# Kernel optimization log

Measured on AMD Instinct MI355X. Metric: run time of the kernel, lower is better.

Reference implementation:

```python
import jax, jax.numpy as jnp
import numpy as np

N_V, N_E, N_F = 6000, 12000, 8000
D_IN, D_OUT = 32, 32


def _glorot(key, shape):
    lim = float(np.sqrt(6.0 / (shape[0] + shape[1])))
    return jax.random.uniform(key, shape, jnp.float32, -lim, lim)


def setup_inputs() -> dict:
    key = jax.random.key(0)
    ks = jax.random.split(key, 13)
    return {
        "xv": jax.random.normal(ks[0], (N_V, D_IN), jnp.float32),
        "xe": jax.random.normal(ks[1], (N_E, D_IN), jnp.float32),
        "xf": jax.random.normal(ks[2], (N_F, D_IN), jnp.float32),
        "Gv2v": jax.random.normal(ks[3], (N_V, N_V), jnp.float32) / np.sqrt(N_V),
        "Gv2e": jax.random.normal(ks[4], (N_E, N_V), jnp.float32) / np.sqrt(N_V),
        "Ge2e": jax.random.normal(ks[5], (N_E, N_E), jnp.float32) / np.sqrt(N_E),
        "Ge2f": jax.random.normal(ks[6], (N_F, N_E), jnp.float32) / np.sqrt(N_E),
        "Gf2f": jax.random.normal(ks[7], (N_F, N_F), jnp.float32) / np.sqrt(N_F),
        "Wv2v": _glorot(ks[8], (D_IN, D_OUT)),
        "Wv2e": _glorot(ks[9], (D_IN, D_OUT)),
        "We2e": _glorot(ks[10], (D_IN, D_OUT)),
        "We2f": _glorot(ks[11], (D_IN, D_OUT)),
        "Wf2f": _glorot(ks[12], (D_IN, D_OUT)),
    }


def reference(xv, xe, xf, Gv2v, Gv2e, Ge2e, Ge2f, Gf2f,
              Wv2v, Wv2e, We2e, We2f, Wf2f):
    # Eval mode: dropout is identity. activation=None -> no nonlinearity.
    # LTN(x, G) = G @ (x @ W); MergeOper = sum of two LTNs.
    zv = Gv2v @ (xv @ Wv2v)                               # [n_v, d_out]
    ze = Gv2e @ (xv @ Wv2e) + Ge2e @ (xe @ We2e)          # [n_e, d_out]
    zf = Ge2f @ (xe @ We2f) + Gf2f @ (xf @ Wf2f)          # [n_f, d_out]
    return zv, ze, zf
```

## Files before the change

kernel.cpp:

```cpp
#include <hip/hip_runtime.h>

typedef float  f32x4 __attribute__((ext_vector_type(4)));
typedef short  s16x8 __attribute__((ext_vector_type(8)));

#define PK   256
#define PSTR 260
#define TM   32

typedef const __attribute__((address_space(1))) float* gas1f;
typedef __attribute__((address_space(3))) float*       las3f;

__device__ __forceinline__ short f2bf(float f) {
  unsigned u = __builtin_bit_cast(unsigned, f);
  u += 0x7FFFu + ((u >> 16) & 1u);
  return (short)(u >> 16);
}

__global__ __launch_bounds__(256) void build_yt(
    const float* __restrict__ xv, const float* __restrict__ xe,
    const float* __restrict__ xf,
    const float* __restrict__ Wv2v, const float* __restrict__ Wv2e,
    const float* __restrict__ We2e, const float* __restrict__ We2f,
    const float* __restrict__ Wf2f, short* __restrict__ Yt)
{
  int bid = blockIdx.x;
  const float* x; const float* W; int K, Kpad; size_t yoff;
  if (bid < 24)       { x=xv; W=Wv2v; K=6000;  Kpad=6144;  yoff=0;       }
  else if (bid < 48)  { x=xv; W=Wv2e; K=6000;  Kpad=6144;  yoff=196608;  bid-=24; }
  else if (bid < 95)  { x=xe; W=We2e; K=12000; Kpad=12032; yoff=393216;  bid-=48; }
  else if (bid < 142) { x=xe; W=We2f; K=12000; Kpad=12032; yoff=778240;  bid-=95; }
  else                { x=xf; W=Wf2f; K=8000;  Kpad=8192;  yoff=1163264; bid-=142; }

  __shared__ float Wl[32][32];
  int tid = threadIdx.x;
  #pragma unroll
  for (int i = 0; i < 4; ++i) {
    int e = tid + i * 256;
    Wl[e >> 5][e & 31] = W[e];
  }
  __syncthreads();

  int row = bid * 256 + tid;
  if (row >= Kpad) return;

  float acc[32];
  #pragma unroll
  for (int c = 0; c < 32; ++c) acc[c] = 0.f;

  if (row < K) {
    const float* xp = x + (size_t)row * 32;
    float xr[32];
    #pragma unroll
    for (int i = 0; i < 8; ++i) {
      f32x4 v = *(const f32x4*)(xp + i * 4);
      xr[i*4+0] = v.x; xr[i*4+1] = v.y; xr[i*4+2] = v.z; xr[i*4+3] = v.w;
    }
    #pragma unroll
    for (int d = 0; d < 32; ++d) {
      float xd = xr[d];
      #pragma unroll
      for (int c = 0; c < 32; ++c) acc[c] += xd * Wl[d][c];
    }
  }
  #pragma unroll
  for (int c = 0; c < 32; ++c)
    Yt[yoff + (size_t)c * Kpad + row] = f2bf(acc[c]);
}

__device__ __forceinline__ void stage_panel(
    const float* __restrict__ G, int K, int row0, int pn, int lane, int w,
    float (*panel)[TM][PSTR], int bb)
{
  if ((pn + 1) * PK <= K) {
    const float* base = G + (size_t)row0 * K + (size_t)pn * PK;
    #pragma unroll
    for (int j = 0; j < 4; ++j) {
      int rr = 4 * w + j;
      __builtin_amdgcn_global_load_lds((gas1f)(base + (size_t)rr * K + lane * 4),
                                       (las3f)&panel[bb][rr][0], 16, 0, 2 );
    }
  } else {
    #pragma unroll
    for (int j = 0; j < 4; ++j) {
      int rr = 4 * w + j;
      int k = pn * PK + lane * 4;
      f32x4 v = {0.f, 0.f, 0.f, 0.f};
      if (k < K) v = *(const f32x4*)(G + (size_t)(row0 + rr) * K + k);
      *(f32x4*)&panel[bb][rr][lane * 4] = v;
    }
  }
}

__device__ __forceinline__ void loadB(const short* __restrict__ Y, int Kp,
                                      int r, int g, int w, int p, s16x8 B[2])
{
  int kg = p * PK + w * 32 + g * 8;
  B[0] = *(const s16x8*)(Y + (size_t)r        * Kp + kg);
  B[1] = *(const s16x8*)(Y + (size_t)(r + 16) * Kp + kg);
}

__device__ __forceinline__ void seg_run(
    const float* __restrict__ G, const short* __restrict__ Yt,
    int K, int Kp, int np, int row0, int lane, int w,
    float (*panel)[TM][PSTR],
    f32x4& acc00, f32x4& acc01, f32x4& acc10, f32x4& acc11)
{
  int r = lane & 15, g = lane >> 4;
  s16x8 Bc[2], Bn[2];

  stage_panel(G, K, row0, 0, lane, w, panel, 0);
  loadB(Yt, Kp, r, g, w, 0, Bc);
  if (np > 1) stage_panel(G, K, row0, 1, lane, w, panel, 1);

  for (int p = 0; p < np; ++p) {
    if (p + 1 < np && (p + 2) * PK <= K)
      asm volatile("s_waitcnt vmcnt(4)" ::: "memory");
    else
      asm volatile("s_waitcnt vmcnt(0)" ::: "memory");
    __builtin_amdgcn_s_barrier();

    int b  = p & 1;
    int kk = w * 32 + g * 8;
    f32x4 l0 = *(const f32x4*)&panel[b][r][kk];
    f32x4 l1 = *(const f32x4*)&panel[b][r][kk + 4];
    f32x4 h0 = *(const f32x4*)&panel[b][r + 16][kk];
    f32x4 h1 = *(const f32x4*)&panel[b][r + 16][kk + 4];
    s16x8 alo, ahi;
    alo[0]=f2bf(l0.x); alo[1]=f2bf(l0.y); alo[2]=f2bf(l0.z); alo[3]=f2bf(l0.w);
    alo[4]=f2bf(l1.x); alo[5]=f2bf(l1.y); alo[6]=f2bf(l1.z); alo[7]=f2bf(l1.w);
    ahi[0]=f2bf(h0.x); ahi[1]=f2bf(h0.y); ahi[2]=f2bf(h0.z); ahi[3]=f2bf(h0.w);
    ahi[4]=f2bf(h1.x); ahi[5]=f2bf(h1.y); ahi[6]=f2bf(h1.z); ahi[7]=f2bf(h1.w);
    acc00 = __builtin_amdgcn_mfma_f32_16x16x32_bf16(alo, Bc[0], acc00, 0, 0, 0);
    acc01 = __builtin_amdgcn_mfma_f32_16x16x32_bf16(alo, Bc[1], acc01, 0, 0, 0);
    acc10 = __builtin_amdgcn_mfma_f32_16x16x32_bf16(ahi, Bc[0], acc10, 0, 0, 0);
    acc11 = __builtin_amdgcn_mfma_f32_16x16x32_bf16(ahi, Bc[1], acc11, 0, 0, 0);

    bool have_next = (p + 1 < np);
    if (have_next) loadB(Yt, Kp, r, g, w, p + 1, Bn);

    asm volatile("s_waitcnt lgkmcnt(0)" ::: "memory");
    __builtin_amdgcn_sched_barrier(0);
    __builtin_amdgcn_s_barrier();
    if (p + 2 < np) stage_panel(G, K, row0, p + 2, lane, w, panel, b);

    if (have_next) { Bc[0] = Bn[0]; Bc[1] = Bn[1]; }
  }
  __syncthreads();
}

__global__ __launch_bounds__(512) void gemm_skinny(
    const float* __restrict__ Gv2v, const float* __restrict__ Gv2e,
    const float* __restrict__ Ge2e, const float* __restrict__ Ge2f,
    const float* __restrict__ Gf2f, const short* __restrict__ Yt,
    float* __restrict__ out)
{
  __shared__ float panel[2][TM][PSTR];

  int bid  = blockIdx.x;
  int lane = threadIdx.x & 63, w = threadIdx.x >> 6;

  const float *G0, *G1; const short *Y0, *Y1;
  int K0, Kp0, n0, K1, Kp1, n1, tile; size_t ob;
  if (bid < 250) {
    tile = bid;
    G0 = Ge2f; Y0 = Yt + 778240;  K0 = 12000; Kp0 = 12032; n0 = 47;
    G1 = Gf2f; Y1 = Yt + 1163264; K1 = 8000;  Kp1 = 8192;  n1 = 32;
    ob = 576000;
  } else if (bid < 625) {
    tile = bid - 250;
    G0 = Gv2e; Y0 = Yt + 196608;  K0 = 6000;  Kp0 = 6144;  n0 = 24;
    G1 = Ge2e; Y1 = Yt + 393216;  K1 = 12000; Kp1 = 12032; n1 = 47;
    ob = 192000;
  } else {
    tile = bid - 625;
    G0 = Gv2v; Y0 = Yt;           K0 = 6000;  Kp0 = 6144;  n0 = 24;
    G1 = nullptr; Y1 = nullptr;   K1 = 0; Kp1 = 0; n1 = 0;
    ob = 0;
  }
  int row0 = tile * TM;
  if (!G1 && row0 + TM > 6000) row0 = 6000 - TM;

  f32x4 acc00 = {0.f,0.f,0.f,0.f}, acc01 = {0.f,0.f,0.f,0.f};
  f32x4 acc10 = {0.f,0.f,0.f,0.f}, acc11 = {0.f,0.f,0.f,0.f};
  seg_run(G0, Y0, K0, Kp0, n0, row0, lane, w, panel, acc00, acc01, acc10, acc11);
  if (G1)
    seg_run(G1, Y1, K1, Kp1, n1, row0, lane, w, panel, acc00, acc01, acc10, acc11);

  float (*red)[1024] = (float (*)[1024])panel;
  int r = lane & 15, g = lane >> 4;
  #pragma unroll
  for (int q = 0; q < 4; ++q) {
    int rl = g * 4 + q;
    red[w][ rl       * 32 +      r] = acc00[q];
    red[w][ rl       * 32 + 16 + r] = acc01[q];
    red[w][(rl + 16) * 32 +      r] = acc10[q];
    red[w][(rl + 16) * 32 + 16 + r] = acc11[q];
  }
  __syncthreads();
  #pragma unroll
  for (int i = 0; i < 2; ++i) {
    int e = (int)threadIdx.x + i * 512;
    float s = red[0][e] + red[1][e] + red[2][e] + red[3][e]
            + red[4][e] + red[5][e] + red[6][e] + red[7][e];
    out[ob + (size_t)row0 * 32 + e] = s;
  }
}

extern "C" void kernel_launch(void* const* d_in, const int* in_sizes, int n_in,
                              void* d_out, int out_size, void* d_ws, size_t ws_size,
                              hipStream_t stream) {
  const float* xv   = (const float*)d_in[0];
  const float* xe   = (const float*)d_in[1];
  const float* xf   = (const float*)d_in[2];
  const float* Gv2v = (const float*)d_in[3];
  const float* Gv2e = (const float*)d_in[4];
  const float* Ge2e = (const float*)d_in[5];
  const float* Ge2f = (const float*)d_in[6];
  const float* Gf2f = (const float*)d_in[7];
  const float* Wv2v = (const float*)d_in[8];
  const float* Wv2e = (const float*)d_in[9];
  const float* We2e = (const float*)d_in[10];
  const float* We2f = (const float*)d_in[11];
  const float* Wf2f = (const float*)d_in[12];
  short* Yt  = (short*)d_ws;
  float* out = (float*)d_out;

  hipLaunchKernelGGL(build_yt, dim3(174), dim3(256), 0, stream,
                     xv, xe, xf, Wv2v, Wv2e, We2e, We2f, Wf2f, Yt);
  hipLaunchKernelGGL(gemm_skinny, dim3(813), dim3(512), 0, stream,
                     Gv2v, Gv2e, Ge2e, Ge2f, Gf2f, Yt, out);
}
```

Baseline: 316.5 us.

## Split-K the long GEMM segments into balanced blocks with a partial-sum reduction

The row tiles of the ze and zf outputs are split along K into two blocks each, with roughly balanced panel counts. One half writes directly to the output and the other writes a partial buffer that a new reduce kernel adds in. The grid grows from 813 to 1438 blocks, which evens out per-block work and the tail. The build_yt transpose writes now go through shared memory so they can be stored as vectors. The cost is an extra kernel launch, extra partial-buffer traffic, and more workspace.

```diff
diff --git a/kernel.cpp b/kernel.cpp
--- a/kernel.cpp
+++ b/kernel.cpp
@@ -32,6 +32,7 @@
   else                { x=xf; W=Wf2f; K=8000;  Kpad=8192;  yoff=1163264; bid-=142; }
 
   __shared__ float Wl[32][32];
+  __shared__ short sh[32][264];
   int tid = threadIdx.x;
   #pragma unroll
   for (int i = 0; i < 4; ++i) {
@@ -41,8 +42,6 @@
   __syncthreads();
 
   int row = bid * 256 + tid;
-  if (row >= Kpad) return;
-
   float acc[32];
   #pragma unroll
   for (int c = 0; c < 32; ++c) acc[c] = 0.f;
@@ -63,8 +62,15 @@
     }
   }
   #pragma unroll
-  for (int c = 0; c < 32; ++c)
-    Yt[yoff + (size_t)c * Kpad + row] = f2bf(acc[c]);
+  for (int c = 0; c < 32; ++c) sh[c][tid] = f2bf(acc[c]);
+  __syncthreads();
+
+  int c = tid >> 3, q = tid & 7;
+  const short* sp = &sh[c][q * 32];
+  short* dp = Yt + yoff + (size_t)c * Kpad + (size_t)bid * 256 + q * 32;
+  #pragma unroll
+  for (int i = 0; i < 4; ++i)
+    *(s16x8*)(dp + i * 8) = *(const s16x8*)(sp + i * 8);
 }
 
 __device__ __forceinline__ void stage_panel(
@@ -101,19 +107,20 @@
 
 __device__ __forceinline__ void seg_run(
     const float* __restrict__ G, const short* __restrict__ Yt,
-    int K, int Kp, int np, int row0, int lane, int w,
+    int K, int Kp, int row0, int p_lo, int p_hi, int lane, int w,
     float (*panel)[TM][PSTR],
     f32x4& acc00, f32x4& acc01, f32x4& acc10, f32x4& acc11)
 {
+  if (p_lo >= p_hi) return;
   int r = lane & 15, g = lane >> 4;
   s16x8 Bc[2], Bn[2];
 
-  stage_panel(G, K, row0, 0, lane, w, panel, 0);
-  loadB(Yt, Kp, r, g, w, 0, Bc);
-  if (np > 1) stage_panel(G, K, row0, 1, lane, w, panel, 1);
-
-  for (int p = 0; p < np; ++p) {
-    if (p + 1 < np && (p + 2) * PK <= K)
+  stage_panel(G, K, row0, p_lo, lane, w, panel, p_lo & 1);
+  loadB(Yt, Kp, r, g, w, p_lo, Bc);
+  if (p_lo + 1 < p_hi) stage_panel(G, K, row0, p_lo + 1, lane, w, panel, (p_lo + 1) & 1);
+
+  for (int p = p_lo; p < p_hi; ++p) {
+    if (p + 1 < p_hi && (p + 2) * PK <= K)
       asm volatile("s_waitcnt vmcnt(4)" ::: "memory");
     else
       asm volatile("s_waitcnt vmcnt(0)" ::: "memory");
@@ -135,13 +142,13 @@
     acc10 = __builtin_amdgcn_mfma_f32_16x16x32_bf16(ahi, Bc[0], acc10, 0, 0, 0);
     acc11 = __builtin_amdgcn_mfma_f32_16x16x32_bf16(ahi, Bc[1], acc11, 0, 0, 0);
 
-    bool have_next = (p + 1 < np);
+    bool have_next = (p + 1 < p_hi);
     if (have_next) loadB(Yt, Kp, r, g, w, p + 1, Bn);
 
     asm volatile("s_waitcnt lgkmcnt(0)" ::: "memory");
     __builtin_amdgcn_sched_barrier(0);
     __builtin_amdgcn_s_barrier();
-    if (p + 2 < np) stage_panel(G, K, row0, p + 2, lane, w, panel, b);
+    if (p + 2 < p_hi) stage_panel(G, K, row0, p + 2, lane, w, panel, b);
 
     if (have_next) { Bc[0] = Bn[0]; Bc[1] = Bn[1]; }
   }
@@ -152,39 +159,48 @@
     const float* __restrict__ Gv2v, const float* __restrict__ Gv2e,
     const float* __restrict__ Ge2e, const float* __restrict__ Ge2f,
     const float* __restrict__ Gf2f, const short* __restrict__ Yt,
-    float* __restrict__ out)
+    float* __restrict__ part, float* __restrict__ out)
 {
   __shared__ float panel[2][TM][PSTR];
 
   int bid  = blockIdx.x;
   int lane = threadIdx.x & 63, w = threadIdx.x >> 6;
 
-  const float *G0, *G1; const short *Y0, *Y1;
-  int K0, Kp0, n0, K1, Kp1, n1, tile; size_t ob;
+  const float *Ga, *Gb = nullptr; const short *Ya, *Yb = nullptr;
+  int Ka, Kpa, alo, ahi, Kb = 0, Kpb = 0, blo = 0, bhi = 0, tile, row0;
+  float* dst;
   if (bid < 250) {
-    tile = bid;
-    G0 = Ge2f; Y0 = Yt + 778240;  K0 = 12000; Kp0 = 12032; n0 = 47;
-    G1 = Gf2f; Y1 = Yt + 1163264; K1 = 8000;  Kp1 = 8192;  n1 = 32;
-    ob = 576000;
-  } else if (bid < 625) {
-    tile = bid - 250;
-    G0 = Gv2e; Y0 = Yt + 196608;  K0 = 6000;  Kp0 = 6144;  n0 = 24;
-    G1 = Ge2e; Y1 = Yt + 393216;  K1 = 12000; Kp1 = 12032; n1 = 47;
-    ob = 192000;
+    tile = bid; row0 = tile * TM;
+    Ga = Ge2f; Ya = Yt + 778240; Ka = 12000; Kpa = 12032; alo = 0;  ahi = 40;
+    dst = out + 576000 + (size_t)tile * 1024;
+  } else if (bid < 500) {
+    tile = bid - 250; row0 = tile * TM;
+    Ga = Ge2f; Ya = Yt + 778240;  Ka = 12000; Kpa = 12032; alo = 40; ahi = 47;
+    Gb = Gf2f; Yb = Yt + 1163264; Kb = 8000;  Kpb = 8192;  blo = 0;  bhi = 32;
+    dst = part + (size_t)tile * 1024;
+  } else if (bid < 875) {
+    tile = bid - 500; row0 = tile * TM;
+    Ga = Ge2e; Ya = Yt + 393216; Ka = 12000; Kpa = 12032; alo = 11; ahi = 47;
+    dst = part + (size_t)(250 + tile) * 1024;
+  } else if (bid < 1250) {
+    tile = bid - 875; row0 = tile * TM;
+    Ga = Gv2e; Ya = Yt + 196608; Ka = 6000;  Kpa = 6144;  alo = 0; ahi = 24;
+    Gb = Ge2e; Yb = Yt + 393216; Kb = 12000; Kpb = 12032; blo = 0; bhi = 11;
+    dst = out + 192000 + (size_t)tile * 1024;
   } else {
-    tile = bid - 625;
-    G0 = Gv2v; Y0 = Yt;           K0 = 6000;  Kp0 = 6144;  n0 = 24;
-    G1 = nullptr; Y1 = nullptr;   K1 = 0; Kp1 = 0; n1 = 0;
-    ob = 0;
-  }
-  int row0 = tile * TM;
-  if (!G1 && row0 + TM > 6000) row0 = 6000 - TM;
+    tile = bid - 1250; row0 = tile * TM;
+    if (row0 + TM > 6000) row0 = 6000 - TM;
+    Ga = Gv2v; Ya = Yt; Ka = 6000; Kpa = 6144; alo = 0; ahi = 24;
+    dst = out + (size_t)row0 * 32;
+  }
 
   f32x4 acc00 = {0.f,0.f,0.f,0.f}, acc01 = {0.f,0.f,0.f,0.f};
   f32x4 acc10 = {0.f,0.f,0.f,0.f}, acc11 = {0.f,0.f,0.f,0.f};
-  seg_run(G0, Y0, K0, Kp0, n0, row0, lane, w, panel, acc00, acc01, acc10, acc11);
-  if (G1)
-    seg_run(G1, Y1, K1, Kp1, n1, row0, lane, w, panel, acc00, acc01, acc10, acc11);
+  seg_run(Ga, Ya, Ka, Kpa, row0, alo, ahi, lane, w, panel,
+          acc00, acc01, acc10, acc11);
+  if (Gb)
+    seg_run(Gb, Yb, Kb, Kpb, row0, blo, bhi, lane, w, panel,
+            acc00, acc01, acc10, acc11);
 
   float (*red)[1024] = (float (*)[1024])panel;
   int r = lane & 15, g = lane >> 4;
@@ -202,7 +218,19 @@
     int e = (int)threadIdx.x + i * 512;
     float s = red[0][e] + red[1][e] + red[2][e] + red[3][e]
             + red[4][e] + red[5][e] + red[6][e] + red[7][e];
-    out[ob + (size_t)row0 * 32 + e] = s;
+    dst[e] = s;
+  }
+}
+
+__global__ __launch_bounds__(256) void reduce_partials(
+    float* __restrict__ out, const float* __restrict__ part)
+{
+  int e = blockIdx.x * 256 + threadIdx.x;
+  if (e < 256000) {
+    out[576000 + e] += part[e];
+  } else {
+    int e2 = e - 256000;
+    out[192000 + e2] += part[256000 + e2];
   }
 }
 
@@ -222,11 +250,14 @@
   const float* We2e = (const float*)d_in[10];
   const float* We2f = (const float*)d_in[11];
   const float* Wf2f = (const float*)d_in[12];
-  short* Yt  = (short*)d_ws;
-  float* out = (float*)d_out;
+  short* Yt   = (short*)d_ws;
+  float* part = (float*)((char*)d_ws + 2850816);
+  float* out  = (float*)d_out;
 
   hipLaunchKernelGGL(build_yt, dim3(174), dim3(256), 0, stream,
                      xv, xe, xf, Wv2v, Wv2e, We2e, We2f, Wf2f, Yt);
-  hipLaunchKernelGGL(gemm_skinny, dim3(813), dim3(512), 0, stream,
-                     Gv2v, Gv2e, Ge2e, Ge2f, Gf2f, Yt, out);
-}
+  hipLaunchKernelGGL(gemm_skinny, dim3(1438), dim3(512), 0, stream,
+                     Gv2v, Gv2e, Ge2e, Ge2f, Gf2f, Yt, part, out);
+  hipLaunchKernelGGL(reduce_partials, dim3(2500), dim3(256), 0, stream,
+                     out, part);
+}
```

Result: faster. 294.9 us (median of 2 runs) (-6.8%).
